# Optimization experiments

Hardware: AMD Instinct MI355X
Metric: run time of the kernel (lower is better)

## Reference

```python
import jax, jax.numpy as jnp
import numpy as np

HEADS = 8
BN_EPS = 1e-5


def setup_inputs() -> dict:
    B, S, D = 8, 1024, 512
    key = jax.random.key(0)
    ks = jax.random.split(key, 4)
    x = jax.random.normal(ks[0], (B, S, D), dtype=jnp.float32)
    scale = 0.02
    Wq = jax.random.normal(ks[1], (D, D), dtype=jnp.float32) * scale
    Wk = jax.random.normal(ks[2], (D, D), dtype=jnp.float32) * scale
    Wv = jax.random.normal(ks[3], (D, D), dtype=jnp.float32) * scale
    zeros = jnp.zeros((D,), dtype=jnp.float32)
    return {
        "x": x,
        "Wq": Wq, "bq": zeros,
        "Wk": Wk, "bk": zeros,
        "Wv": Wv, "bv": zeros,
        "gamma": jnp.ones((D,), dtype=jnp.float32),
        "beta": zeros,
    }


def reference(x, Wq, bq, Wk, bk, Wv, bv, gamma, beta):
    # x: [B, S, D]
    B, S, D = x.shape
    H = HEADS
    dh = D // H

    Q = jax.nn.relu(jnp.einsum('bsd,de->bse', x, Wq) + bq).reshape(B, S, H, dh)
    K = jax.nn.relu(jnp.einsum('bsd,de->bse', x, Wk) + bk).reshape(B, S, H, dh)
    V = jax.nn.relu(jnp.einsum('bsd,de->bse', x, Wv) + bv).reshape(B, S, H, dh)

    # torch split(dim=2)+cat(dim=0) == per-head batched attention; scores [B,H,q,k]
    scores = jnp.einsum('bqhd,bkhd->bhqk', Q, K) / jnp.sqrt(jnp.float32(dh))
    # NOTE: original uses F.softmax(output, dim=1) on [H*B, S, S]; dim=1 is the
    # QUERY axis (non-standard), i.e. axis 2 of [b,h,q,k].
    attn = jax.nn.softmax(scores, axis=2)
    # dropout omitted (deterministic / eval mode)
    out = jnp.einsum('bhqk,bkhd->bqhd', attn, V).reshape(B, S, D)

    y = out + x  # residual

    # BatchNorm1d (training mode): per-channel stats over (B, S), biased var
    mean = jnp.mean(y, axis=(0, 1))
    var = jnp.mean(jnp.square(y - mean), axis=(0, 1))
    y = (y - mean) * jax.lax.rsqrt(var + BN_EPS) * gamma + beta
    return y
```

## Files before the change

### kernel.cpp

```cpp
#include <hip/hip_runtime.h>
#include <hip/hip_bf16.h>
#include <math.h>

typedef __bf16 bf16;
typedef __bf16 bf16x8 __attribute__((ext_vector_type(8)));
typedef float floatx4 __attribute__((ext_vector_type(4)));

#define NB 8
#define NS 1024
#define ND 512
#define NH 8
#define NDH 64
#define NBH 64
#define MROWS 8192
#define N3 1536
#define KSCL 0.18033688f

#define GLD16(src, dst)                                                            \
    __builtin_amdgcn_global_load_lds(                                              \
        (const __attribute__((address_space(1))) void*)(src),                      \
        (__attribute__((address_space(3))) void*)(dst), 16, 0, 0)

static __device__ __forceinline__ floatx4 mfma16(bf16x8 a, bf16x8 b, floatx4 c) {
    return __builtin_amdgcn_mfma_f32_16x16x32_bf16(a, b, c, 0, 0, 0);
}

static __device__ __forceinline__ float fexp2(float x) {
#if __has_builtin(__builtin_amdgcn_exp2f)
    return __builtin_amdgcn_exp2f(x);
#else
    return __expf(x * 0.69314718f);
#endif
}

static __device__ __forceinline__ unsigned pack2(float lo, float hi) {
    union { bf16 h[2]; unsigned u; } u;
    u.h[0] = (bf16)lo; u.h[1] = (bf16)hi;
    return u.u;
}

static __device__ __forceinline__ void plane32(unsigned &a, unsigned &b) {
    asm("v_permlane32_swap_b32 %0, %1" : "+v"(a), "+v"(b));
}
static __device__ __forceinline__ void plane16(unsigned &a, unsigned &b) {
    asm("v_permlane16_swap_b32 %0, %1" : "+v"(a), "+v"(b));
}

__global__ void prep(const float* __restrict__ x, bf16* __restrict__ xb,
                     float* __restrict__ bnSum, const float* __restrict__ Wq,
                     const float* __restrict__ Wk, const float* __restrict__ Wv,
                     bf16* __restrict__ Wb) {
    __shared__ float tl[32][33];
    int bid = blockIdx.x;
    int t = threadIdx.x;
    if (bid < 2048) {
        if (bid == 0) {
            ((float4*)bnSum)[t] = make_float4(0.f, 0.f, 0.f, 0.f);
        }
        int i = (bid * 256 + t) * 8;
        float4 a = *(const float4*)&x[i];
        float4 b = *(const float4*)&x[i + 4];
        bf16 o[8] = {(bf16)a.x, (bf16)a.y, (bf16)a.z, (bf16)a.w,
                     (bf16)b.x, (bf16)b.y, (bf16)b.z, (bf16)b.w};
        *(bf16x8*)&xb[i] = *(bf16x8*)o;
    } else {
        int wbid = bid - 2048;
        int mat = wbid >> 8;
        int bx = wbid & 15;
        int by = (wbid >> 4) & 15;
        const float* W = mat == 0 ? Wq : (mat == 1 ? Wk : Wv);
        int d0 = bx * 32, e0 = by * 32;
        int tx = t & 31, ty = t >> 5;
#pragma unroll
        for (int i = 0; i < 4; i++) tl[ty * 4 + i][tx] = W[(d0 + ty * 4 + i) * ND + e0 + tx];
        __syncthreads();
#pragma unroll
        for (int i = 0; i < 4; i++)
            Wb[(mat * ND + e0 + ty * 4 + i) * ND + d0 + tx] = (bf16)tl[tx][ty * 4 + i];
    }
}

__launch_bounds__(256)
__global__ void gemm1(const bf16* __restrict__ xb, const bf16* __restrict__ Wb,
                      const float* __restrict__ bq, const float* __restrict__ bk,
                      const float* __restrict__ bv, bf16* __restrict__ QKV) {
    __shared__ __align__(16) bf16 As[128 * 64];
    __shared__ __align__(16) bf16 Bs[128 * 64];
    int t = threadIdx.x, lane = t & 63, w = t >> 6;
    int wr = w >> 1, wc = w & 1;
    int lr = lane & 15, lg = lane >> 4;
    int row0 = blockIdx.x * 128, col0 = blockIdx.y * 128;
    int srow = t >> 3, sj = t & 7;
    floatx4 acc[4][4] = {};
    for (int k0 = 0; k0 < ND; k0 += 64) {
        __syncthreads();
#pragma unroll
        for (int it = 0; it < 4; it++) {
            int row = it * 32 + srow;
            int j = sj ^ (row & 7);
            GLD16(&xb[(size_t)(row0 + row) * ND + k0 + j * 8], &As[(it * 256 + w * 64) * 8]);
            GLD16(&Wb[(size_t)(col0 + row) * ND + k0 + j * 8], &Bs[(it * 256 + w * 64) * 8]);
        }
        __syncthreads();
        bf16x8 af[2][4], bfr[2][4];
#pragma unroll
        for (int ks = 0; ks < 2; ks++) {
#pragma unroll
            for (int mt = 0; mt < 4; mt++)
                af[ks][mt] = *(const bf16x8*)&As[(wr * 64 + mt * 16 + lr) * 64 +
                                                 ((ks * 4 + lg) ^ (lr & 7)) * 8];
#pragma unroll
            for (int nt = 0; nt < 4; nt++)
                bfr[ks][nt] = *(const bf16x8*)&Bs[(wc * 64 + nt * 16 + lr) * 64 +
                                                  ((ks * 4 + lg) ^ (lr & 7)) * 8];
        }
#pragma unroll
        for (int ks = 0; ks < 2; ks++)
#pragma unroll
            for (int mt = 0; mt < 4; mt++)
#pragma unroll
                for (int nt = 0; nt < 4; nt++)
                    acc[mt][nt] = mfma16(af[ks][mt], bfr[ks][nt], acc[mt][nt]);
    }
#pragma unroll
    for (int mt = 0; mt < 4; mt++)
#pragma unroll
        for (int nt = 0; nt < 4; nt++) {
            int col = col0 + wc * 64 + nt * 16 + lr;
            float bias = col < 512 ? bq[col] : (col < 1024 ? bk[col - 512] : bv[col - 1024]);
            float scl = (col >= 512 && col < 1024) ? KSCL : 1.0f;
#pragma unroll
            for (int r = 0; r < 4; r++) {
                int row = row0 + wr * 64 + mt * 16 + lg * 4 + r;
                float v = acc[mt][nt][r] + bias;
                v = v > 0.f ? v : 0.f;
                v *= scl;
                QKV[(size_t)row * N3 + col] = (bf16)v;
            }
        }
}

__launch_bounds__(256)
__global__ void attn_colsum_vt(const bf16* __restrict__ QKV, bf16* __restrict__ Vt) {
    __shared__ __align__(16) bf16 Qs[128 * 64];
    __shared__ float rcS[128];
    int bh = blockIdx.x, b = bh >> 3, h = bh & 7;
    int k0 = blockIdx.y * 128;
    int t = threadIdx.x, lane = t & 63, w = t >> 6;
    int lr = lane & 15, lg = lane >> 4;
    int srow = t >> 3, sj = t & 7;
    bf16x8 kf[2][2];
#pragma unroll
    for (int tt = 0; tt < 2; tt++)
#pragma unroll
        for (int s = 0; s < 2; s++)
            kf[tt][s] = *(const bf16x8*)&QKV[(size_t)(b * NS + k0 + w * 32 + tt * 16 + lr) * N3 +
                                             512 + h * NDH + s * 32 + lg * 8];
    floatx4 csum[2] = {};
    const floatx4 zf = {};
    for (int qc = 0; qc < 8; qc++) {
        __syncthreads();
#pragma unroll
        for (int it = 0; it < 4; it++) {
            int row = it * 32 + srow;
            int j = sj ^ (row & 7);
            GLD16(&QKV[(size_t)(b * NS + qc * 128 + row) * N3 + h * NDH + j * 8],
                  &Qs[(it * 256 + w * 64) * 8]);
        }
        __syncthreads();
        __builtin_amdgcn_s_setprio(1);
#pragma unroll
        for (int qt = 0; qt < 8; qt++) {
            bf16x8 qb0 = *(const bf16x8*)&Qs[(qt * 16 + lr) * 64 + (lg ^ (lr & 7)) * 8];
            bf16x8 qb1 = *(const bf16x8*)&Qs[(qt * 16 + lr) * 64 + ((4 + lg) ^ (lr & 7)) * 8];
#pragma unroll
            for (int tt = 0; tt < 2; tt++) {
                floatx4 a = mfma16(kf[tt][0], qb0, zf);
                a = mfma16(kf[tt][1], qb1, a);
#pragma unroll
                for (int r = 0; r < 4; r++) csum[tt][r] += fexp2(a[r]);
            }
        }
        __builtin_amdgcn_s_setprio(0);
    }
#pragma unroll
    for (int tt = 0; tt < 2; tt++)
#pragma unroll
        for (int r = 0; r < 4; r++) {
            float v = csum[tt][r];
            v += __shfl_xor(v, 1);
            v += __shfl_xor(v, 2);
            v += __shfl_xor(v, 4);
            v += __shfl_xor(v, 8);
            csum[tt][r] = v;
        }
    if (lr == 0) {
#pragma unroll
        for (int tt = 0; tt < 2; tt++)
#pragma unroll
            for (int r = 0; r < 4; r++)
                rcS[w * 32 + tt * 16 + lg * 4 + r] = 1.f / csum[tt][r];
    }
    __syncthreads();
#pragma unroll
    for (int it = 0; it < 4; it++) {
        int row = it * 32 + srow;
        int j = sj ^ (row & 7);
        GLD16(&QKV[(size_t)(b * NS + k0 + row) * N3 + 1024 + h * NDH + j * 8],
              &Qs[(it * 256 + w * 64) * 8]);
    }
    __syncthreads();
    int d = lane;
#pragma unroll
    for (int c = 0; c < 4; c++) {
        int s0l = (w * 4 + c) * 8;
        bf16 tmp[8];
#pragma unroll
        for (int j = 0; j < 8; j++) {
            int row = s0l + j;
            float v = (float)Qs[row * 64 + (((d >> 3) ^ (row & 7)) * 8) + (d & 7)];
            tmp[j] = (bf16)(v * rcS[row]);
        }
        *(bf16x8*)&Vt[(size_t)(bh * NDH + d) * NS + k0 + s0l] = *(bf16x8*)tmp;
    }
}

__launch_bounds__(256)
__global__ void attn_fused(bf16* __restrict__ QKV, const bf16* __restrict__ Vt,
                           const float* __restrict__ x,
                           float* __restrict__ bnSum, float* __restrict__ bnSumSq) {
    __shared__ __align__(16) bf16 Ks[128 * 64];
    __shared__ __align__(16) bf16 Vs[64 * 128];
    int bh = blockIdx.x, b = bh >> 3, h = bh & 7;
    int q0 = blockIdx.y * 128;
    int t = threadIdx.x, lane = t & 63, w = t >> 6;
    int lr = lane & 15, lg = lane >> 4;
    bf16x8 qf[2][2];
#pragma unroll
    for (int n = 0; n < 2; n++)
#pragma unroll
        for (int s = 0; s < 2; s++)
            qf[n][s] = *(const bf16x8*)&QKV[(size_t)(b * NS + q0 + w * 32 + n * 16 + lr) * N3 +
                                            h * NDH + s * 32 + lg * 8];
    int sKrow = t >> 3, sKj = t & 7;
    int sVrow = t >> 4, sVj = t & 15;
    floatx4 oacc[2][4] = {};
    const floatx4 zf = {};
    for (int kb = 0; kb < 8; kb++) {
        int k0 = kb * 128;
        __syncthreads();
#pragma unroll
        for (int it = 0; it < 4; it++) {
            int rowK = it * 32 + sKrow;
            int jK = sKj ^ (rowK & 7);
            GLD16(&QKV[(size_t)(b * NS + k0 + rowK) * N3 + 512 + h * NDH + jK * 8],
                  &Ks[(it * 256 + w * 64) * 8]);
            int rowV = it * 16 + sVrow;
            int jV = sVj ^ (rowV & 7);
            GLD16(&Vt[(size_t)(bh * NDH + rowV) * NS + k0 + jV * 8],
                  &Vs[(it * 256 + w * 64) * 8]);
        }
        __syncthreads();
        __builtin_amdgcn_s_setprio(1);
#pragma unroll
        for (int kt = 0; kt < 4; kt++) {
            bf16x8 kfr[2][2];
#pragma unroll
            for (int tt = 0; tt < 2; tt++)
#pragma unroll
                for (int s = 0; s < 2; s++)
                    kfr[tt][s] = *(const bf16x8*)&Ks[(kt * 32 + tt * 16 + lr) * 64 +
                                                     ((s * 4 + lg) ^ (lr & 7)) * 8];
            bf16x8 vf[4];
#pragma unroll
            for (int nt = 0; nt < 4; nt++)
                vf[nt] = *(const bf16x8*)&Vs[(nt * 16 + lr) * 128 +
                                             ((kt * 4 + lg) ^ (lr & 7)) * 8];
#pragma unroll
            for (int n = 0; n < 2; n++) {
                floatx4 s0 = mfma16(kfr[0][0], qf[n][0], zf);
                s0 = mfma16(kfr[0][1], qf[n][1], s0);
                floatx4 s1 = mfma16(kfr[1][0], qf[n][0], zf);
                s1 = mfma16(kfr[1][1], qf[n][1], s1);
                float e0[4], e1[4];
#pragma unroll
                for (int r = 0; r < 4; r++) {
                    e0[r] = fexp2(s0[r]);
                    e1[r] = fexp2(s1[r]);
                }
                unsigned A0 = pack2(e0[0], e0[1]);
                unsigned A1 = pack2(e0[2], e0[3]);
                unsigned B0 = pack2(e1[0], e1[1]);
                unsigned B1 = pack2(e1[2], e1[3]);
                plane32(A0, B0); plane16(A0, B0);
                plane32(A1, B1); plane16(A1, B1);
                union { unsigned u[4]; bf16x8 v; } af;
                af.u[0] = A0; af.u[1] = A1; af.u[2] = B0; af.u[3] = B1;
#pragma unroll
                for (int nt = 0; nt < 4; nt++)
                    oacc[n][nt] = mfma16(af.v, vf[nt], oacc[n][nt]);
            }
        }
        __builtin_amdgcn_s_setprio(0);
    }
    float bs[4] = {}, bq2[4] = {};
#pragma unroll
    for (int n = 0; n < 2; n++)
#pragma unroll
        for (int nt = 0; nt < 4; nt++) {
            int d = nt * 16 + lr;
#pragma unroll
            for (int r = 0; r < 4; r++) {
                int q = q0 + w * 32 + n * 16 + lg * 4 + r;
                size_t row = (size_t)(b * NS + q);
                float yv = oacc[n][nt][r] + x[row * ND + h * NDH + d];
                QKV[row * N3 + 1024 + h * NDH + d] = (bf16)yv;
                bs[nt] += yv;
                bq2[nt] += yv * yv;
            }
        }
#pragma unroll
    for (int nt = 0; nt < 4; nt++) {
        float v = bs[nt], q2 = bq2[nt];
        v += __shfl_xor(v, 16); v += __shfl_xor(v, 32);
        q2 += __shfl_xor(q2, 16); q2 += __shfl_xor(q2, 32);
        if (lg == 0) {
            atomicAdd(&bnSum[h * NDH + nt * 16 + lr], v);
            atomicAdd(&bnSumSq[h * NDH + nt * 16 + lr], q2);
        }
    }
}

__global__ void bn_apply(const bf16* __restrict__ QKV, float* __restrict__ y,
                         const float* __restrict__ bnSum, const float* __restrict__ bnSumSq,
                         const float* __restrict__ gamma, const float* __restrict__ beta) {
    int i = (blockIdx.x * 256 + threadIdx.x) * 8;
    int row = i >> 9, col = i & 511;
    bf16x8 yv = *(const bf16x8*)&QKV[(size_t)row * N3 + 1024 + col];
    float4 s0 = *(const float4*)&bnSum[col];
    float4 s1 = *(const float4*)&bnSum[col + 4];
    float4 q0 = *(const float4*)&bnSumSq[col];
    float4 q1 = *(const float4*)&bnSumSq[col + 4];
    float4 g0 = *(const float4*)&gamma[col];
    float4 g1 = *(const float4*)&gamma[col + 4];
    float4 b0 = *(const float4*)&beta[col];
    float4 b1 = *(const float4*)&beta[col + 4];
    float sm[8] = {s0.x, s0.y, s0.z, s0.w, s1.x, s1.y, s1.z, s1.w};
    float sq[8] = {q0.x, q0.y, q0.z, q0.w, q1.x, q1.y, q1.z, q1.w};
    float gm[8] = {g0.x, g0.y, g0.z, g0.w, g1.x, g1.y, g1.z, g1.w};
    float bt[8] = {b0.x, b0.y, b0.z, b0.w, b1.x, b1.y, b1.z, b1.w};
    float out[8];
#pragma unroll
    for (int j = 0; j < 8; j++) {
        float mean = sm[j] * (1.f / 8192.f);
        float var = sq[j] * (1.f / 8192.f) - mean * mean;
        float rstd = rsqrtf(var + 1e-5f);
        out[j] = ((float)yv[j] - mean) * rstd * gm[j] + bt[j];
    }
    *(float4*)&y[i] = make_float4(out[0], out[1], out[2], out[3]);
    *(float4*)&y[i + 4] = make_float4(out[4], out[5], out[6], out[7]);
}

extern "C" void kernel_launch(void* const* d_in, const int* in_sizes, int n_in,
                              void* d_out, int out_size, void* d_ws, size_t ws_size,
                              hipStream_t stream) {
    const float* x  = (const float*)d_in[0];
    const float* Wq = (const float*)d_in[1];
    const float* bq = (const float*)d_in[2];
    const float* Wk = (const float*)d_in[3];
    const float* bk = (const float*)d_in[4];
    const float* Wv = (const float*)d_in[5];
    const float* bv = (const float*)d_in[6];
    const float* gamma = (const float*)d_in[7];
    const float* beta  = (const float*)d_in[8];
    float* y = (float*)d_out;

    char* ws = (char*)d_ws;
    const size_t WB_OFF  = 0;
    const size_t QKV_OFF = 2u << 20;
    const size_t VT_OFF  = QKV_OFF + (size_t)MROWS * N3 * 2;
    const size_t BN_OFF  = VT_OFF + (size_t)NBH * NDH * NS * 2;
    const size_t XB_OFF  = BN_OFF + (4u << 12);
    bf16*  Wb     = (bf16*)(ws + WB_OFF);
    bf16*  QKV    = (bf16*)(ws + QKV_OFF);
    bf16*  Vt     = (bf16*)(ws + VT_OFF);
    float* bnSum  = (float*)(ws + BN_OFF);
    float* bnSumSq = bnSum + 512;
    bf16*  xb     = (bf16*)(ws + XB_OFF);

    prep<<<2816, 256, 0, stream>>>(x, xb, bnSum, Wq, Wk, Wv, Wb);
    gemm1<<<dim3(64, 12), 256, 0, stream>>>(xb, Wb, bq, bk, bv, QKV);
    attn_colsum_vt<<<dim3(64, 8), 256, 0, stream>>>(QKV, Vt);
    attn_fused<<<dim3(64, 8), 256, 0, stream>>>(QKV, Vt, x, bnSum, bnSumSq);
    bn_apply<<<2048, 256, 0, stream>>>(QKV, y, bnSum, bnSumSq, gamma, beta);
}
```

Baseline: 82.58 us.

## Store scaled V in MFMA fragment-blob layout and load directly from global

```diff
diff --git a/kernel.cpp b/kernel.cpp
--- a/kernel.cpp
+++ b/kernel.cpp
@@ -141,7 +141,7 @@
 }
 
 __launch_bounds__(256)
-__global__ void attn_colsum_vt(const bf16* __restrict__ QKV, bf16* __restrict__ Vt) {
+__global__ void attn_colsum_vt(const bf16* __restrict__ QKV, bf16* __restrict__ VB) {
     __shared__ __align__(16) bf16 Qs[128 * 64];
     __shared__ float rcS[128];
     int bh = blockIdx.x, b = bh >> 3, h = bh & 7;
@@ -210,27 +210,26 @@
               &Qs[(it * 256 + w * 64) * 8]);
     }
     __syncthreads();
-    int d = lane;
-#pragma unroll
-    for (int c = 0; c < 4; c++) {
-        int s0l = (w * 4 + c) * 8;
+#pragma unroll
+    for (int nt = 0; nt < 4; nt++) {
+        int d = nt * 16 + lr;
         bf16 tmp[8];
 #pragma unroll
         for (int j = 0; j < 8; j++) {
-            int row = s0l + j;
+            int row = w * 32 + lg * 8 + j;
             float v = (float)Qs[row * 64 + (((d >> 3) ^ (row & 7)) * 8) + (d & 7)];
             tmp[j] = (bf16)(v * rcS[row]);
         }
-        *(bf16x8*)&Vt[(size_t)(bh * NDH + d) * NS + k0 + s0l] = *(bf16x8*)tmp;
+        size_t blob = (size_t)((bh * 32 + (k0 >> 5) + w) * 4 + nt);
+        *(bf16x8*)&VB[blob * 512 + lane * 8] = *(bf16x8*)tmp;
     }
 }
 
 __launch_bounds__(256)
-__global__ void attn_fused(bf16* __restrict__ QKV, const bf16* __restrict__ Vt,
+__global__ void attn_fused(bf16* __restrict__ QKV, const bf16* __restrict__ VB,
                            const float* __restrict__ x,
                            float* __restrict__ bnSum, float* __restrict__ bnSumSq) {
     __shared__ __align__(16) bf16 Ks[128 * 64];
-    __shared__ __align__(16) bf16 Vs[64 * 128];
     int bh = blockIdx.x, b = bh >> 3, h = bh & 7;
     int q0 = blockIdx.y * 128;
     int t = threadIdx.x, lane = t & 63, w = t >> 6;
@@ -242,8 +241,8 @@
         for (int s = 0; s < 2; s++)
             qf[n][s] = *(const bf16x8*)&QKV[(size_t)(b * NS + q0 + w * 32 + n * 16 + lr) * N3 +
                                             h * NDH + s * 32 + lg * 8];
+    const bf16* vbase = &VB[(size_t)(bh * 32) * 4 * 512 + lane * 8];
     int sKrow = t >> 3, sKj = t & 7;
-    int sVrow = t >> 4, sVj = t & 15;
     floatx4 oacc[2][4] = {};
     const floatx4 zf = {};
     for (int kb = 0; kb < 8; kb++) {
@@ -255,10 +254,6 @@
             int jK = sKj ^ (rowK & 7);
             GLD16(&QKV[(size_t)(b * NS + k0 + rowK) * N3 + 512 + h * NDH + jK * 8],
                   &Ks[(it * 256 + w * 64) * 8]);
-            int rowV = it * 16 + sVrow;
-            int jV = sVj ^ (rowV & 7);
-            GLD16(&Vt[(size_t)(bh * NDH + rowV) * NS + k0 + jV * 8],
-                  &Vs[(it * 256 + w * 64) * 8]);
         }
         __syncthreads();
         __builtin_amdgcn_s_setprio(1);
@@ -274,8 +269,7 @@
             bf16x8 vf[4];
 #pragma unroll
             for (int nt = 0; nt < 4; nt++)
-                vf[nt] = *(const bf16x8*)&Vs[(nt * 16 + lr) * 128 +
-                                             ((kt * 4 + lg) ^ (lr & 7)) * 8];
+                vf[nt] = *(const bf16x8*)&vbase[(size_t)((kb * 4 + kt) * 4 + nt) * 512];
 #pragma unroll
             for (int n = 0; n < 2; n++) {
                 floatx4 s0 = mfma16(kfr[0][0], qf[n][0], zf);
@@ -383,14 +377,14 @@
     const size_t XB_OFF  = BN_OFF + (4u << 12);
     bf16*  Wb     = (bf16*)(ws + WB_OFF);
     bf16*  QKV    = (bf16*)(ws + QKV_OFF);
-    bf16*  Vt     = (bf16*)(ws + VT_OFF);
+    bf16*  VB     = (bf16*)(ws + VT_OFF);
     float* bnSum  = (float*)(ws + BN_OFF);
     float* bnSumSq = bnSum + 512;
     bf16*  xb     = (bf16*)(ws + XB_OFF);
 
     prep<<<2816, 256, 0, stream>>>(x, xb, bnSum, Wq, Wk, Wv, Wb);
     gemm1<<<dim3(64, 12), 256, 0, stream>>>(xb, Wb, bq, bk, bv, QKV);
-    attn_colsum_vt<<<dim3(64, 8), 256, 0, stream>>>(QKV, Vt);
-    attn_fused<<<dim3(64, 8), 256, 0, stream>>>(QKV, Vt, x, bnSum, bnSumSq);
+    attn_colsum_vt<<<dim3(64, 8), 256, 0, stream>>>(QKV, VB);
+    attn_fused<<<dim3(64, 8), 256, 0, stream>>>(QKV, VB, x, bnSum, bnSumSq);
     bn_apply<<<2048, 256, 0, stream>>>(QKV, y, bnSum, bnSumSq, gamma, beta);
 }
```

Result: no change. 81.86 us (median of 2 runs) (-0.9%).
